# Optimization experiments

Hardware: AMD Instinct MI355X
Metric: run time of the kernel (lower is better)

The kernel has to match this reference:

```python
import jax, jax.numpy as jnp
import numpy as np

N_NODES = 50000
N_EDGES = 600000
NODE_DIM = 128
HIDDEN = 128
LN_EPS = 1e-5


def setup_inputs() -> dict:
    key = jax.random.key(0)
    ks = jax.random.split(key, 12)
    x = jax.random.normal(ks[0], (N_NODES, NODE_DIM), dtype=jnp.float32)
    edge_index = jax.random.randint(ks[1], (2, N_EDGES), 0, N_NODES, dtype=jnp.int32)
    # GCNConv weights (glorot-ish scaling)
    W1 = jax.random.normal(ks[2], (NODE_DIM, HIDDEN), dtype=jnp.float32) / np.sqrt(NODE_DIM)
    b1 = jnp.zeros((HIDDEN,), jnp.float32)
    W2 = jax.random.normal(ks[3], (HIDDEN, HIDDEN), dtype=jnp.float32) / np.sqrt(HIDDEN)
    b2 = jnp.zeros((HIDDEN,), jnp.float32)
    g1 = jnp.ones((HIDDEN,), jnp.float32)
    beta1 = jnp.zeros((HIDDEN,), jnp.float32)
    g2 = jnp.ones((HIDDEN,), jnp.float32)
    beta2 = jnp.zeros((HIDDEN,), jnp.float32)
    return {"x": x, "edge_index": edge_index, "W1": W1, "b1": b1, "g1": g1,
            "beta1": beta1, "W2": W2, "b2": b2, "g2": g2, "beta2": beta2}


def _gcn_conv(x, src, dst, norm, W, b, n):
    # x' = sum_{j->i} norm_ji * (x_j @ W) + b   (self-loops already in src/dst)
    h = x @ W                                   # [N, H]
    msg = h[src] * norm[:, None]                # [E+N, H]
    out = jax.ops.segment_sum(msg, dst, num_segments=n)
    return out + b


def _layer_norm(x, gamma, beta):
    mu = jnp.mean(x, axis=-1, keepdims=True)
    var = jnp.mean((x - mu) ** 2, axis=-1, keepdims=True)
    return (x - mu) * jax.lax.rsqrt(var + LN_EPS) * gamma + beta


def reference(x, edge_index, W1, b1, g1, beta1, W2, b2, g2, beta2):
    n = x.shape[0]
    loop = jnp.arange(n, dtype=edge_index.dtype)
    src = jnp.concatenate([edge_index[0], loop])
    dst = jnp.concatenate([edge_index[1], loop])
    # symmetric normalization with self-loops (PyG GCNConv default)
    deg = jax.ops.segment_sum(jnp.ones_like(dst, dtype=x.dtype), dst, num_segments=n)
    dinv = jnp.where(deg > 0, jax.lax.rsqrt(jnp.maximum(deg, 1.0)), 0.0)
    norm = dinv[src] * dinv[dst]                # [E+N]

    h = _gcn_conv(x, src, dst, norm, W1, b1, n)
    h = _layer_norm(h, g1, beta1)
    h = jax.nn.relu(h)                          # relu between layers only
    h = _gcn_conv(h, src, dst, norm, W2, b2, n)
    h = _layer_norm(h, g2, beta2)
    return h
```

## Files before the change

kernel.cpp:

```cpp
#include <hip/hip_runtime.h>

#define DIM 128
#define LN_EPS 1e-5f

typedef __attribute__((ext_vector_type(8))) short bf16x8;
typedef __attribute__((ext_vector_type(4))) float f32x4;

static __device__ __forceinline__ unsigned short f2bf(float f) {
    unsigned int u = __builtin_bit_cast(unsigned int, f);
    u += 0x7fffu + ((u >> 16) & 1u);
    return (unsigned short)(u >> 16);
}
static __device__ __forceinline__ float bf2f_lo(unsigned int u) {
    return __builtin_bit_cast(float, u << 16);
}
static __device__ __forceinline__ float bf2f_hi(unsigned int u) {
    return __builtin_bit_cast(float, u & 0xffff0000u);
}

__global__ __launch_bounds__(256) void wt_count_kernel(const float* __restrict__ W1,
                                                       const float* __restrict__ W2,
                                                       unsigned short* __restrict__ Wt1,
                                                       unsigned short* __restrict__ Wt2,
                                                       const int* __restrict__ dst,
                                                       int* __restrict__ counts, int E) {
    int b = blockIdx.x;
    if (b < 128) {
        int elem = b * 256 + threadIdx.x;
        int which = elem >> 14;
        int rest = elem & 16383;
        int c = rest >> 7;
        int k = rest & 127;
        const float* W = which ? W2 : W1;
        unsigned short* Wt = which ? Wt2 : Wt1;
        Wt[c * 128 + k] = f2bf(W[k * 128 + c]);
    } else {
        int e = (b - 128) * 256 + threadIdx.x;
        if (e < E) atomicAdd(&counts[dst[e]], 1);
    }
}

__global__ __launch_bounds__(256) void scan1_kernel(const int* __restrict__ counts,
                                                    int* __restrict__ tmp,
                                                    int* __restrict__ bsums,
                                                    float* __restrict__ dinv, int n) {
    __shared__ int ts[256];
    int tid = threadIdx.x;
    int base = blockIdx.x * 1024 + tid * 4;
    int v[4];
#pragma unroll
    for (int j = 0; j < 4; ++j) {
        int i = base + j;
        v[j] = (i < n) ? counts[i] : 0;
        if (i < n) dinv[i] = rsqrtf((float)(v[j] + 1));
    }
    int s = v[0] + v[1] + v[2] + v[3];
    ts[tid] = s;
    __syncthreads();
    for (int off = 1; off < 256; off <<= 1) {
        int t2 = (tid >= off) ? ts[tid - off] : 0;
        __syncthreads();
        ts[tid] += t2;
        __syncthreads();
    }
    int excl = ts[tid] - s;
    int pre = excl;
#pragma unroll
    for (int j = 0; j < 4; ++j) {
        int i = base + j;
        if (i < n) tmp[i] = pre;
        pre += v[j];
    }
    if (tid == 255) bsums[blockIdx.x] = ts[255];
}

__global__ __launch_bounds__(256) void scan3_kernel(const int* __restrict__ tmp,
                                                    const int* __restrict__ bsums,
                                                    int* __restrict__ rowptr,
                                                    int* __restrict__ cursor,
                                                    int n, int E, int nb) {
    __shared__ int s_add;
    if (threadIdx.x < 64) {
        int lane = threadIdx.x;
        int v = (lane < nb) ? bsums[lane] : 0;
        int x = v;
#pragma unroll
        for (int off = 1; off < 64; off <<= 1) {
            int y = __shfl_up(x, off);
            if (lane >= off) x += y;
        }
        int excl = x - v;
        int mine = __builtin_amdgcn_readlane(excl, blockIdx.x);
        if (lane == 0) s_add = mine;
    }
    __syncthreads();
    int add = s_add;
    int base = blockIdx.x * 1024 + threadIdx.x * 4;
#pragma unroll
    for (int j = 0; j < 4; ++j) {
        int i = base + j;
        if (i < n) {
            int val = tmp[i] + add;
            rowptr[i] = val;
            cursor[i] = val;
        }
    }
    if (blockIdx.x == 0 && threadIdx.x == 0) rowptr[n] = E;
}

__global__ __launch_bounds__(256) void fill_kernel(const int* __restrict__ src,
                                                   const int* __restrict__ dst,
                                                   int* __restrict__ cursor,
                                                   unsigned short* __restrict__ colsrc, int E) {
    int e = blockIdx.x * 256 + threadIdx.x;
    if (e < E) {
        int p = atomicAdd(&cursor[dst[e]], 1);
        colsrc[p] = (unsigned short)src[e];
    }
}

__global__ __launch_bounds__(256) void gemm_mfma_f32_kernel(const float* __restrict__ A,
                                                            const unsigned short* __restrict__ Bt,
                                                            const float* __restrict__ dinv,
                                                            unsigned short* __restrict__ H,
                                                            int n, int ntiles) {
    __shared__ unsigned short Wlds[128 * 136];
    for (int u = threadIdx.x; u < 2048; u += 256) {
        int row = u >> 4;
        int sub = u & 15;
        *(bf16x8*)&Wlds[row * 136 + sub * 8] = *(const bf16x8*)(Bt + row * 128 + sub * 8);
    }
    __syncthreads();

    int wid = threadIdx.x >> 6;
    int lane = threadIdx.x & 63;
    int tile = blockIdx.x * 4 + wid;
    if (tile >= ntiles) tile = ntiles - 1;
    int r0 = tile * 16;
    int mrow = lane & 15;
    int kgrp = lane >> 4;

    int arow_i = r0 + mrow;
    if (arow_i > n - 1) arow_i = n - 1;
    const float* arow = A + (size_t)arow_i * DIM + kgrp * 8;

    f32x4 acc[8];
#pragma unroll
    for (int t = 0; t < 8; ++t) acc[t] = (f32x4){0.f, 0.f, 0.f, 0.f};

#pragma unroll
    for (int kc = 0; kc < 4; ++kc) {
        float4 v0 = *(const float4*)(arow + kc * 32);
        float4 v1 = *(const float4*)(arow + kc * 32 + 4);
        bf16x8 af;
        af[0] = (short)f2bf(v0.x); af[1] = (short)f2bf(v0.y);
        af[2] = (short)f2bf(v0.z); af[3] = (short)f2bf(v0.w);
        af[4] = (short)f2bf(v1.x); af[5] = (short)f2bf(v1.y);
        af[6] = (short)f2bf(v1.z); af[7] = (short)f2bf(v1.w);
#pragma unroll
        for (int t = 0; t < 8; ++t) {
            bf16x8 bfv = *(const bf16x8*)&Wlds[(t * 16 + mrow) * 136 + kc * 32 + kgrp * 8];
            acc[t] = __builtin_amdgcn_mfma_f32_16x16x32_bf16(af, bfv, acc[t], 0, 0, 0);
        }
    }

    float dv[4];
#pragma unroll
    for (int reg = 0; reg < 4; ++reg) {
        int rr = r0 + kgrp * 4 + reg;
        dv[reg] = (rr < n) ? dinv[rr] : 0.f;
    }
#pragma unroll
    for (int t = 0; t < 8; ++t) {
#pragma unroll
        for (int reg = 0; reg < 4; ++reg) {
            int row = r0 + kgrp * 4 + reg;
            if (row < n) {
                int col = t * 16 + mrow;
                H[(size_t)row * DIM + col] = f2bf(acc[t][reg] * dv[reg]);
            }
        }
    }
}

__global__ __launch_bounds__(256) void gemm_mfma_kernel(const unsigned short* __restrict__ A,
                                                        const unsigned short* __restrict__ Bt,
                                                        const float* __restrict__ dinv,
                                                        unsigned short* __restrict__ H,
                                                        int n, int ntiles) {
    __shared__ unsigned short Wlds[128 * 136];
    for (int u = threadIdx.x; u < 2048; u += 256) {
        int row = u >> 4;
        int sub = u & 15;
        *(bf16x8*)&Wlds[row * 136 + sub * 8] = *(const bf16x8*)(Bt + row * 128 + sub * 8);
    }
    __syncthreads();

    int wid = threadIdx.x >> 6;
    int lane = threadIdx.x & 63;
    int tile = blockIdx.x * 4 + wid;
    if (tile >= ntiles) tile = ntiles - 1;
    int r0 = tile * 16;
    int mrow = lane & 15;
    int kgrp = lane >> 4;

    int arow_i = r0 + mrow;
    if (arow_i > n - 1) arow_i = n - 1;
    const unsigned short* arow = A + (size_t)arow_i * DIM + kgrp * 8;

    f32x4 acc[8];
#pragma unroll
    for (int t = 0; t < 8; ++t) acc[t] = (f32x4){0.f, 0.f, 0.f, 0.f};

#pragma unroll
    for (int kc = 0; kc < 4; ++kc) {
        bf16x8 af = *(const bf16x8*)(arow + kc * 32);
#pragma unroll
        for (int t = 0; t < 8; ++t) {
            bf16x8 bfv = *(const bf16x8*)&Wlds[(t * 16 + mrow) * 136 + kc * 32 + kgrp * 8];
            acc[t] = __builtin_amdgcn_mfma_f32_16x16x32_bf16(af, bfv, acc[t], 0, 0, 0);
        }
    }

    float dv[4];
#pragma unroll
    for (int reg = 0; reg < 4; ++reg) {
        int rr = r0 + kgrp * 4 + reg;
        dv[reg] = (rr < n) ? dinv[rr] : 0.f;
    }
#pragma unroll
    for (int t = 0; t < 8; ++t) {
#pragma unroll
        for (int reg = 0; reg < 4; ++reg) {
            int row = r0 + kgrp * 4 + reg;
            if (row < n) {
                int col = t * 16 + mrow;
                H[(size_t)row * DIM + col] = f2bf(acc[t][reg] * dv[reg]);
            }
        }
    }
}

__global__ __launch_bounds__(256) void gather_ln_kernel(const int* __restrict__ rowptr,
                                                        const unsigned short* __restrict__ colsrc,
                                                        const unsigned int* __restrict__ Hb,
                                                        const float* __restrict__ dinv,
                                                        const float* __restrict__ bias,
                                                        const float* __restrict__ gamma,
                                                        const float* __restrict__ beta,
                                                        unsigned int* __restrict__ out_bf,
                                                        float* __restrict__ out_f,
                                                        int n, int relu) {
    int wid = threadIdx.x >> 6;
    int lane = threadIdx.x & 63;
    int r = blockIdx.x * 4 + wid;
    if (r >= n) return;

    float di = dinv[r];
    float2 bb = ((const float2*)bias)[lane];
    float2 gg = ((const float2*)gamma)[lane];
    float2 be = ((const float2*)beta)[lane];

    unsigned int su = Hb[(size_t)r * 64 + lane];
    float ax = bf2f_lo(su), ay = bf2f_hi(su);

    int p = rowptr[r];
    int p1 = rowptr[r + 1];
    while (p < p1) {
        int cnt = p1 - p;
        if (cnt > 16) cnt = 16;
        int gi = p + lane;
        gi = gi < p1 ? gi : p1 - 1;
        int idxv = (int)colsrc[gi];

        unsigned int h[16];
#pragma unroll
        for (int j = 0; j < 16; ++j) {
            int s = __builtin_amdgcn_readlane(idxv, j);
            h[j] = Hb[(size_t)s * 64 + lane];
        }

#pragma unroll
        for (int j = 0; j < 16; ++j) {
            bool act = (j < cnt);
            ax += act ? bf2f_lo(h[j]) : 0.f;
            ay += act ? bf2f_hi(h[j]) : 0.f;
        }
        p += cnt;
    }

    float vx = ax * di + bb.x;
    float vy = ay * di + bb.y;

    float s1 = vx + vy;
    float s2 = vx * vx + vy * vy;
#pragma unroll
    for (int off = 32; off > 0; off >>= 1) {
        s1 += __shfl_xor(s1, off);
        s2 += __shfl_xor(s2, off);
    }
    float mu = s1 * (1.f / 128.f);
    float var = s2 * (1.f / 128.f) - mu * mu;
    float rstd = rsqrtf(var + LN_EPS);

    float ox = (vx - mu) * rstd * gg.x + be.x;
    float oy = (vy - mu) * rstd * gg.y + be.y;
    if (relu) {
        ox = fmaxf(ox, 0.f);
        oy = fmaxf(oy, 0.f);
    }
    if (out_bf) {
        unsigned int pk = (unsigned int)f2bf(ox) | ((unsigned int)f2bf(oy) << 16);
        out_bf[(size_t)r * 64 + lane] = pk;
    } else {
        ((float2*)out_f)[(size_t)r * 64 + lane] = make_float2(ox, oy);
    }
}

extern "C" void kernel_launch(void* const* d_in, const int* in_sizes, int n_in,
                              void* d_out, int out_size, void* d_ws, size_t ws_size,
                              hipStream_t stream) {
    const float* x   = (const float*)d_in[0];
    const int*   ei  = (const int*)d_in[1];
    const float* W1  = (const float*)d_in[2];
    const float* b1  = (const float*)d_in[3];
    const float* g1  = (const float*)d_in[4];
    const float* be1 = (const float*)d_in[5];
    const float* W2  = (const float*)d_in[6];
    const float* b2  = (const float*)d_in[7];
    const float* g2  = (const float*)d_in[8];
    const float* be2 = (const float*)d_in[9];

    int n = in_sizes[0] / DIM;
    int E = in_sizes[1] / 2;
    const int* src = ei;
    const int* dst = ei + E;

    char* wp = (char*)d_ws;
    auto alloc = [&](size_t bytes) {
        void* p = (void*)wp;
        wp += (bytes + 255) & ~(size_t)255;
        return p;
    };
    float*          dinv   = (float*)alloc((size_t)n * 4);
    int*            counts = (int*)alloc((size_t)n * 4);
    int*            tmp    = (int*)alloc((size_t)n * 4);
    int*            rowptr = (int*)alloc((size_t)(n + 1) * 4);
    int*            cursor = (int*)alloc((size_t)n * 4);
    int*            bsums  = (int*)alloc(64 * 4);
    unsigned short* colsrc = (unsigned short*)alloc((size_t)E * 2);
    unsigned short* Wt1    = (unsigned short*)alloc(128 * 128 * 2);
    unsigned short* Wt2    = (unsigned short*)alloc(128 * 128 * 2);
    unsigned short* H      = (unsigned short*)alloc((size_t)n * DIM * 2);
    unsigned short* Y1     = (unsigned short*)alloc((size_t)n * DIM * 2);

    hipMemsetAsync(counts, 0, (size_t)n * 4, stream);

    int gE = (E + 255) / 256;
    wt_count_kernel<<<128 + gE, 256, 0, stream>>>(W1, W2, Wt1, Wt2, dst, counts, E);

    int nb1 = (n + 1023) / 1024;
    scan1_kernel<<<nb1, 256, 0, stream>>>(counts, tmp, bsums, dinv, n);
    scan3_kernel<<<nb1, 256, 0, stream>>>(tmp, bsums, rowptr, cursor, n, E, nb1);
    fill_kernel<<<gE, 256, 0, stream>>>(src, dst, cursor, colsrc, E);

    int ntiles = (n + 15) / 16;
    int gG = (ntiles + 3) / 4;
    int gA = (n + 3) / 4;

    gemm_mfma_f32_kernel<<<gG, 256, 0, stream>>>(x, Wt1, dinv, H, n, ntiles);
    gather_ln_kernel<<<gA, 256, 0, stream>>>(rowptr, colsrc, (const unsigned int*)H, dinv,
                                             b1, g1, be1, (unsigned int*)Y1, nullptr, n, 1);

    gemm_mfma_kernel<<<gG, 256, 0, stream>>>(Y1, Wt2, dinv, H, n, ntiles);
    gather_ln_kernel<<<gA, 256, 0, stream>>>(rowptr, colsrc, (const unsigned int*)H, dinv,
                                             b2, g2, be2, nullptr, (float*)d_out, n, 0);
}
```

Measured before the change: 234.9 us.

## Process two rows per wavefront in gather-LN with 8-byte loads per lane

Each 64-lane wavefront now handles two nodes, with a half-wave of 32 lanes per row. Each lane loads 4 bf16 values (uint2) instead of 2 and uses float4 for bias, gamma and beta. The LN reduction shrinks to a 32-lane shuffle, and neighbor indices are broadcast with shfl instead of readlane. This aims to raise memory-level parallelism and cut per-row overhead, but both halves iterate to the larger degree of the two rows, which wastes work on the shorter one.

```diff
diff --git a/kernel.cpp b/kernel.cpp
--- a/kernel.cpp
+++ b/kernel.cpp
@@ -243,59 +243,69 @@
 
 __global__ __launch_bounds__(256) void gather_ln_kernel(const int* __restrict__ rowptr,
                                                         const unsigned short* __restrict__ colsrc,
-                                                        const unsigned int* __restrict__ Hb,
+                                                        const uint2* __restrict__ H2,
                                                         const float* __restrict__ dinv,
                                                         const float* __restrict__ bias,
                                                         const float* __restrict__ gamma,
                                                         const float* __restrict__ beta,
-                                                        unsigned int* __restrict__ out_bf,
+                                                        uint2* __restrict__ out_bf,
                                                         float* __restrict__ out_f,
                                                         int n, int relu) {
     int wid = threadIdx.x >> 6;
     int lane = threadIdx.x & 63;
-    int r = blockIdx.x * 4 + wid;
-    if (r >= n) return;
-
-    float di = dinv[r];
-    float2 bb = ((const float2*)bias)[lane];
-    float2 gg = ((const float2*)gamma)[lane];
-    float2 be = ((const float2*)beta)[lane];
-
-    unsigned int su = Hb[(size_t)r * 64 + lane];
-    float ax = bf2f_lo(su), ay = bf2f_hi(su);
-
-    int p = rowptr[r];
-    int p1 = rowptr[r + 1];
-    while (p < p1) {
-        int cnt = p1 - p;
-        if (cnt > 16) cnt = 16;
-        int gi = p + lane;
+    int half = lane >> 5;
+    int hl = lane & 31;
+    int r = blockIdx.x * 8 + wid * 2 + half;
+    int valid = (r < n);
+    int rc = valid ? r : (n - 1);
+
+    float di = dinv[rc];
+    float4 bb = ((const float4*)bias)[hl];
+    float4 gg = ((const float4*)gamma)[hl];
+    float4 be = ((const float4*)beta)[hl];
+
+    uint2 su = H2[(size_t)rc * 32 + hl];
+    float a0 = bf2f_lo(su.x), a1 = bf2f_hi(su.x);
+    float a2 = bf2f_lo(su.y), a3 = bf2f_hi(su.y);
+
+    int p0 = rowptr[rc];
+    int p1 = rowptr[rc + 1];
+    int deg = p1 - p0;
+    int maxd = max(deg, __shfl_xor(deg, 32));
+    int nchunks = (maxd + 15) >> 4;
+    int hbase = half << 5;
+
+    for (int c = 0; c < nchunks; ++c) {
+        int cbase = c * 16;
+        int gi = p0 + cbase + hl;
         gi = gi < p1 ? gi : p1 - 1;
         int idxv = (int)colsrc[gi];
 
-        unsigned int h[16];
+        uint2 h[16];
 #pragma unroll
         for (int j = 0; j < 16; ++j) {
-            int s = __builtin_amdgcn_readlane(idxv, j);
-            h[j] = Hb[(size_t)s * 64 + lane];
-        }
-
+            int s = __shfl(idxv, hbase + j);
+            h[j] = H2[(size_t)s * 32 + hl];
+        }
 #pragma unroll
         for (int j = 0; j < 16; ++j) {
-            bool act = (j < cnt);
-            ax += act ? bf2f_lo(h[j]) : 0.f;
-            ay += act ? bf2f_hi(h[j]) : 0.f;
-        }
-        p += cnt;
-    }
-
-    float vx = ax * di + bb.x;
-    float vy = ay * di + bb.y;
-
-    float s1 = vx + vy;
-    float s2 = vx * vx + vy * vy;
-#pragma unroll
-    for (int off = 32; off > 0; off >>= 1) {
+            bool act = (cbase + j < deg);
+            a0 += act ? bf2f_lo(h[j].x) : 0.f;
+            a1 += act ? bf2f_hi(h[j].x) : 0.f;
+            a2 += act ? bf2f_lo(h[j].y) : 0.f;
+            a3 += act ? bf2f_hi(h[j].y) : 0.f;
+        }
+    }
+
+    float v0 = a0 * di + bb.x;
+    float v1 = a1 * di + bb.y;
+    float v2 = a2 * di + bb.z;
+    float v3 = a3 * di + bb.w;
+
+    float s1 = v0 + v1 + v2 + v3;
+    float s2 = v0 * v0 + v1 * v1 + v2 * v2 + v3 * v3;
+#pragma unroll
+    for (int off = 16; off > 0; off >>= 1) {
         s1 += __shfl_xor(s1, off);
         s2 += __shfl_xor(s2, off);
     }
@@ -303,17 +313,23 @@
     float var = s2 * (1.f / 128.f) - mu * mu;
     float rstd = rsqrtf(var + LN_EPS);
 
-    float ox = (vx - mu) * rstd * gg.x + be.x;
-    float oy = (vy - mu) * rstd * gg.y + be.y;
+    float o0 = (v0 - mu) * rstd * gg.x + be.x;
+    float o1 = (v1 - mu) * rstd * gg.y + be.y;
+    float o2 = (v2 - mu) * rstd * gg.z + be.z;
+    float o3 = (v3 - mu) * rstd * gg.w + be.w;
     if (relu) {
-        ox = fmaxf(ox, 0.f);
-        oy = fmaxf(oy, 0.f);
-    }
-    if (out_bf) {
-        unsigned int pk = (unsigned int)f2bf(ox) | ((unsigned int)f2bf(oy) << 16);
-        out_bf[(size_t)r * 64 + lane] = pk;
-    } else {
-        ((float2*)out_f)[(size_t)r * 64 + lane] = make_float2(ox, oy);
+        o0 = fmaxf(o0, 0.f); o1 = fmaxf(o1, 0.f);
+        o2 = fmaxf(o2, 0.f); o3 = fmaxf(o3, 0.f);
+    }
+    if (valid) {
+        if (out_bf) {
+            uint2 pk;
+            pk.x = (unsigned int)f2bf(o0) | ((unsigned int)f2bf(o1) << 16);
+            pk.y = (unsigned int)f2bf(o2) | ((unsigned int)f2bf(o3) << 16);
+            out_bf[(size_t)r * 32 + hl] = pk;
+        } else {
+            ((float4*)out_f)[(size_t)r * 32 + hl] = make_float4(o0, o1, o2, o3);
+        }
     }
 }
 
@@ -366,13 +382,13 @@
 
     int ntiles = (n + 15) / 16;
     int gG = (ntiles + 3) / 4;
-    int gA = (n + 3) / 4;
+    int gA = (n + 7) / 8;
 
     gemm_mfma_f32_kernel<<<gG, 256, 0, stream>>>(x, Wt1, dinv, H, n, ntiles);
-    gather_ln_kernel<<<gA, 256, 0, stream>>>(rowptr, colsrc, (const unsigned int*)H, dinv,
-                                             b1, g1, be1, (unsigned int*)Y1, nullptr, n, 1);
+    gather_ln_kernel<<<gA, 256, 0, stream>>>(rowptr, colsrc, (const uint2*)H, dinv,
+                                             b1, g1, be1, (uint2*)Y1, nullptr, n, 1);
 
     gemm_mfma_kernel<<<gG, 256, 0, stream>>>(Y1, Wt2, dinv, H, n, ntiles);
-    gather_ln_kernel<<<gA, 256, 0, stream>>>(rowptr, colsrc, (const unsigned int*)H, dinv,
+    gather_ln_kernel<<<gA, 256, 0, stream>>>(rowptr, colsrc, (const uint2*)H, dinv,
                                              b2, g2, be2, nullptr, (float*)d_out, n, 0);
 }
```

Measured after the change: 232.5 us. Within noise of the previous version (-1.1%).
